# Performance work log

Hardware: AMD Instinct MI355X
Metric: run time of the kernel (lower is better)

The kernel has to match this reference:

```python
import jax, jax.numpy as jnp
import numpy as np

C = 192
NUM_HEADS = 4
K = 3
KV_STRIDE = 2
EPS = 1e-5


def _conv(x, w, stride, groups):
    # x: [B,C,H,W], w: [O, I//groups, kh, kw]
    return jax.lax.conv_general_dilated(
        x, w, window_strides=(stride, stride),
        padding=[(K // 2, K // 2), (K // 2, K // 2)] if w.shape[-1] > 1 else [(0, 0), (0, 0)],
        dimension_numbers=("NCHW", "OIHW", "NCHW"),
        feature_group_count=groups)


def _bn(x, gamma, beta, mean, var):
    # eval-mode batchnorm over channel dim of NCHW
    inv = gamma / jnp.sqrt(var + EPS)
    return x * inv[None, :, None, None] + (beta - mean * inv)[None, :, None, None]


def _dwconv_flatten(x, dw, g, b, m, v, pw, stride):
    y = _conv(x, dw, stride, groups=C)          # depthwise
    y = _bn(y, g, b, m, v)
    y = _conv(y, pw, 1, groups=1)               # 1x1 pointwise
    B, O, h, w = y.shape
    return y.reshape(B, O, h * w).transpose(0, 2, 1)  # b (h w) c


def setup_inputs() -> dict:
    key = jax.random.key(0)
    ks = jax.random.split(key, 16)
    B, H, W = 8, 56, 56
    d = {
        "x": jax.random.normal(ks[0], (B, H * W, C), jnp.float32),
        "H": H,
        "W": W,
        "dw_q": jax.random.normal(ks[1], (C, 1, K, K), jnp.float32) * 0.1,
        "bn_q_gamma": jax.random.uniform(ks[2], (C,), jnp.float32, 0.5, 1.5),
        "bn_q_beta": jax.random.normal(ks[3], (C,), jnp.float32) * 0.1,
        "bn_q_mean": jax.random.normal(ks[4], (C,), jnp.float32) * 0.1,
        "bn_q_var": jax.random.uniform(ks[5], (C,), jnp.float32, 0.5, 1.5),
        "pw_q": jax.random.normal(ks[6], (C, C, 1, 1), jnp.float32) * (1.0 / np.sqrt(C)),
        "dw_kv": jax.random.normal(ks[7], (C, 1, K, K), jnp.float32) * 0.1,
        "bn_kv_gamma": jax.random.uniform(ks[8], (C,), jnp.float32, 0.5, 1.5),
        "bn_kv_beta": jax.random.normal(ks[9], (C,), jnp.float32) * 0.1,
        "bn_kv_mean": jax.random.normal(ks[10], (C,), jnp.float32) * 0.1,
        "bn_kv_var": jax.random.uniform(ks[11], (C,), jnp.float32, 0.5, 1.5),
        "pw_kv": jax.random.normal(ks[12], (2 * C, C, 1, 1), jnp.float32) * (1.0 / np.sqrt(C)),
        "Wq": jax.random.normal(ks[13], (C, C), jnp.float32) * (1.0 / np.sqrt(C)),
        "bq": jnp.zeros((C,), jnp.float32),
        "Wk": jax.random.normal(ks[14], (C, C), jnp.float32) * (1.0 / np.sqrt(C)),
        "bk": jnp.zeros((C,), jnp.float32),
        "Wv": jax.random.normal(ks[15], (C, C), jnp.float32) * (1.0 / np.sqrt(C)),
        "bv": jnp.zeros((C,), jnp.float32),
    }
    return d


def reference(x, H, W, dw_q, bn_q_gamma, bn_q_beta, bn_q_mean, bn_q_var, pw_q,
              dw_kv, bn_kv_gamma, bn_kv_beta, bn_kv_mean, bn_kv_var, pw_kv,
              Wq, bq, Wk, bk, Wv, bv):
    B, N, _ = x.shape
    h = NUM_HEADS
    hd = C // h
    scale = hd ** -0.5
    # Token2Patch: b (H W) c -> b c H W
    xp = x.transpose(0, 2, 1).reshape(B, C, H, W)
    conv_q = _dwconv_flatten(xp, dw_q, bn_q_gamma, bn_q_beta, bn_q_mean, bn_q_var, pw_q, 1)  # [B,N,C]
    kv = _dwconv_flatten(xp, dw_kv, bn_kv_gamma, bn_kv_beta, bn_kv_mean, bn_kv_var, pw_kv, KV_STRIDE)  # [B,M,2C]
    conv_k, conv_v = kv[..., :C], kv[..., C:]
    q = (conv_q @ Wq.T + bq).reshape(B, N, h, hd).transpose(0, 2, 1, 3)      # [B,h,N,hd]
    M = conv_k.shape[1]
    k = (conv_k @ Wk.T + bk).reshape(B, M, h, hd).transpose(0, 2, 1, 3)      # [B,h,M,hd]
    v = (conv_v @ Wv.T + bv).reshape(B, M, h, hd).transpose(0, 2, 1, 3)      # [B,h,M,hd]
    attn = jnp.einsum("bhnd,bhmd->bhnm", q, k) * scale
    attn = jax.nn.softmax(attn, axis=-1)
    out = jnp.einsum("bhnm,bhmd->bhnd", attn, v)
    # MergeHeads: b h n d -> b n (h d)
    return out.transpose(0, 2, 1, 3).reshape(B, N, C)
```

## Files before the change

kernel.cpp:

```cpp
#include <hip/hip_runtime.h>
#include <cmath>

typedef _Float16 f16;
typedef _Float16 f16x8 __attribute__((ext_vector_type(8)));
typedef _Float16 f16x4 __attribute__((ext_vector_type(4)));
typedef float    f32x4 __attribute__((ext_vector_type(4)));
typedef unsigned int u32;
typedef u32 u32x2 __attribute__((ext_vector_type(2)));

#define C_   192
#define HH   56
#define WW   56
#define NN   3136
#define BB   8
#define MM   784
#define NHEAD 4
#define HD   48
#define VT_LD 832
#define QPB  (BB*NN/32)
#define KVPB (BB*MM/32)

#define MFMA16(a,b,c)  __builtin_amdgcn_mfma_f32_16x16x32_f16(a,b,c,0,0,0)
#define MFMAK16(a,b,c) __builtin_amdgcn_mfma_f32_16x16x16f16(a,b,c,0,0,0)

static __device__ __forceinline__ u32 pkrtz(float a, float b) {
    typedef __fp16 fp16x2 __attribute__((ext_vector_type(2)));
    fp16x2 h = __builtin_amdgcn_cvt_pkrtz(a, b);
    return __builtin_bit_cast(u32, h);
}

static __device__ __forceinline__ void gload16(const void* g, void* l) {
    __builtin_amdgcn_global_load_lds(
        (const __attribute__((address_space(1))) unsigned int*)g,
        (__attribute__((address_space(3))) unsigned int*)l, 16, 0, 0);
}

template<int STRIDE, int OH, int OW>
__device__ __forceinline__ void dwbn_quad(
    const float* __restrict__ x, const float* __restrict__ dwL,
    const float* __restrict__ gamma, const float* __restrict__ beta,
    const float* __restrict__ mean,  const float* __restrict__ var,
    f16* __restrict__ out, int idx)
{
    int c4 = idx % 48;
    int r1 = idx / 48;
    int qx = r1 % (OW/2);
    int r2 = r1 / (OW/2);
    int qp = r2 % (OH/2);
    int b  = r2 / (OH/2);
    int c0 = c4*4;

    float4 w4[9];
    #pragma unroll
    for (int j = 0; j < 9; ++j)
        w4[j] = *(const float4*)&dwL[c4*40 + j*4];
    const float* wf = (const float*)w4;

    float4 g4  = *(const float4*)(gamma + c0);
    float4 be4 = *(const float4*)(beta + c0);
    float4 m4  = *(const float4*)(mean + c0);
    float4 v4  = *(const float4*)(var  + c0);

    float4 a00 = make_float4(0.f,0.f,0.f,0.f);
    float4 a01 = a00, a10 = a00, a11 = a00;
    int iyTop = (2*qp)*STRIDE - 1;
    int ix0   = (2*qx)*STRIDE - 1;
    #pragma unroll
    for (int j = 0; j < STRIDE+3; ++j) {
        int iy = iyTop + j;
        if (iy < 0 || iy >= HH) continue;
        #pragma unroll
        for (int i = 0; i < STRIDE+3; ++i) {
            int ix = ix0 + i;
            if (ix < 0 || ix >= WW) continue;
            float4 xv = *reinterpret_cast<const float4*>(
                x + ((size_t)b*NN + iy*WW + ix)*C_ + c0);
            const bool r0ok = (j <= 2), r1ok = (j >= STRIDE);
            const bool c0ok = (i <= 2), c1ok = (i >= STRIDE);
            if (r0ok && c0ok) { const int wi = j*3 + i;
                a00.x = fmaf(wf[ 0+wi], xv.x, a00.x);
                a00.y = fmaf(wf[ 9+wi], xv.y, a00.y);
                a00.z = fmaf(wf[18+wi], xv.z, a00.z);
                a00.w = fmaf(wf[27+wi], xv.w, a00.w); }
            if (r0ok && c1ok) { const int wi = j*3 + (i-STRIDE);
                a01.x = fmaf(wf[ 0+wi], xv.x, a01.x);
                a01.y = fmaf(wf[ 9+wi], xv.y, a01.y);
                a01.z = fmaf(wf[18+wi], xv.z, a01.z);
                a01.w = fmaf(wf[27+wi], xv.w, a01.w); }
            if (r1ok && c0ok) { const int wi = (j-STRIDE)*3 + i;
                a10.x = fmaf(wf[ 0+wi], xv.x, a10.x);
                a10.y = fmaf(wf[ 9+wi], xv.y, a10.y);
                a10.z = fmaf(wf[18+wi], xv.z, a10.z);
                a10.w = fmaf(wf[27+wi], xv.w, a10.w); }
            if (r1ok && c1ok) { const int wi = (j-STRIDE)*3 + (i-STRIDE);
                a11.x = fmaf(wf[ 0+wi], xv.x, a11.x);
                a11.y = fmaf(wf[ 9+wi], xv.y, a11.y);
                a11.z = fmaf(wf[18+wi], xv.z, a11.z);
                a11.w = fmaf(wf[27+wi], xv.w, a11.w); }
        }
    }
    float i0 = g4.x*__frsqrt_rn(v4.x + 1e-5f);
    float i1 = g4.y*__frsqrt_rn(v4.y + 1e-5f);
    float i2 = g4.z*__frsqrt_rn(v4.z + 1e-5f);
    float i3 = g4.w*__frsqrt_rn(v4.w + 1e-5f);
    float b0 = be4.x - m4.x*i0, b1 = be4.y - m4.y*i1;
    float b2 = be4.z - m4.z*i2, b3 = be4.w - m4.w*i3;
    size_t base = (((size_t)b*OH + 2*qp)*OW + 2*qx)*48 + c4;
    f16x4 r;
    r[0]=(f16)(a00.x*i0+b0); r[1]=(f16)(a00.y*i1+b1);
    r[2]=(f16)(a00.z*i2+b2); r[3]=(f16)(a00.w*i3+b3);
    *reinterpret_cast<f16x4*>(out + base*4) = r;
    r[0]=(f16)(a01.x*i0+b0); r[1]=(f16)(a01.y*i1+b1);
    r[2]=(f16)(a01.z*i2+b2); r[3]=(f16)(a01.w*i3+b3);
    *reinterpret_cast<f16x4*>(out + (base + 48)*4) = r;
    r[0]=(f16)(a10.x*i0+b0); r[1]=(f16)(a10.y*i1+b1);
    r[2]=(f16)(a10.z*i2+b2); r[3]=(f16)(a10.w*i3+b3);
    *reinterpret_cast<f16x4*>(out + (base + (size_t)OW*48)*4) = r;
    r[0]=(f16)(a11.x*i0+b0); r[1]=(f16)(a11.y*i1+b1);
    r[2]=(f16)(a11.z*i2+b2); r[3]=(f16)(a11.w*i3+b3);
    *reinterpret_cast<f16x4*>(out + (base + (size_t)OW*48 + 48)*4) = r;
}

__global__ __launch_bounds__(256) void prep_all(
    const float* __restrict__ x,
    const float* __restrict__ dwq,  const float* __restrict__ gq,
    const float* __restrict__ bq_,  const float* __restrict__ mq,
    const float* __restrict__ vq,
    const float* __restrict__ dwkv, const float* __restrict__ gkv,
    const float* __restrict__ bkv,  const float* __restrict__ mkv,
    const float* __restrict__ vkv,
    const float* __restrict__ Wq, const float* __restrict__ Wk,
    const float* __restrict__ Wv, const float* __restrict__ pw_q,
    const float* __restrict__ pw_kv,
    f16* __restrict__ uq, f16* __restrict__ ukv,
    f16* __restrict__ Mq, f16* __restrict__ Mk, f16* __restrict__ Mv,
    f16* __restrict__ vt)
{
    int blk = blockIdx.x, tid = threadIdx.x;
    const int QB = 1176, KB = 294;
    if (blk < QB + KB) {
        bool qp = blk < QB;
        __shared__ __align__(16) float dwL[48*40];
        const float* dwg = qp ? dwq : dwkv;
        for (int i = tid; i < 432; i += 256) {
            int f  = i*4;
            int c4 = f/36, r = f%36;
            *(float4*)&dwL[c4*40 + r] = *(const float4*)(dwg + f);
        }
        __syncthreads();
        if (qp)
            dwbn_quad<1, HH, WW>(x, dwL, gq, bq_, mq, vq, uq, blk*256 + tid);
        else
            dwbn_quad<2, 28, 28>(x, dwL, gkv, bkv, mkv, vkv, ukv,
                                 (blk - QB)*256 + tid);
    } else if (blk < QB + KB + 576) {
        int fb = blk - QB - KB;
        int which = fb / 192, o = fb % 192;
        const float* Wm = which == 0 ? Wq : (which == 1 ? Wk : Wv);
        const float* P  = which == 0 ? pw_q : (which == 1 ? pw_kv : pw_kv + C_*C_);
        f16* Mo         = which == 0 ? Mq : (which == 1 ? Mk : Mv);
        __shared__ float wrow[C_];
        if (tid < C_) wrow[tid] = Wm[o*C_ + tid];
        __syncthreads();
        if (tid < C_) {
            float acc = 0.f;
            #pragma unroll 8
            for (int j = 0; j < C_; ++j)
                acc = fmaf(wrow[j], P[j*C_ + tid], acc);
            Mo[o*C_ + tid] = (f16)acc;
        }
    } else {
        int i = (blk - QB - KB - 576)*256 + tid;
        int b = i / (C_*48);
        int rem = i % (C_*48);
        int c = rem / 48;
        int m = MM + (rem % 48);
        vt[((size_t)b*C_ + c)*VT_LD + m] = (f16)0.f;
    }
}

__global__ __launch_bounds__(128, 1) void proj_all(
    const f16* __restrict__ uq, const f16* __restrict__ ukv,
    const f16* __restrict__ Mq, const f16* __restrict__ Mk,
    const f16* __restrict__ Mv,
    const float* __restrict__ bq, const float* __restrict__ bk,
    const float* __restrict__ bv,
    f16* __restrict__ qb, f16* __restrict__ kb, f16* __restrict__ vt)
{
    int tid  = threadIdx.x;
    int w    = tid >> 6, l = tid & 63;
    int lrow = l & 15,  lgrp = l >> 4;
    int blk  = blockIdx.x;
    int path = blk < QPB ? 0 : (blk < QPB + KVPB ? 1 : 2);
    const f16* U = path == 0 ? uq : ukv;
    int rblk = path == 0 ? blk : (path == 1 ? blk - QPB : blk - QPB - KVPB);
    int r0 = rblk*32 + w*16;

    const f16* urow = U + (size_t)(r0 + lrow)*C_;
    f16x8 a[6];
    #pragma unroll
    for (int ch = 0; ch < 6; ++ch)
        a[ch] = *(const f16x8*)(urow + ch*32 + lgrp*8);

    f16x8 bfA[6], bfB[6];
    const f16* Mm = path == 0 ? Mq : (path == 1 ? Mk : Mv);

    #pragma unroll
    for (int ch = 0; ch < 6; ++ch)
        bfA[ch] = *(const f16x8*)(Mm + (size_t)lrow*C_ + ch*32 + lgrp*8);

    if (path < 2) {
        const float sc = path == 0 ? 0.14433756729740643f*1.4426950408889634f
                                   : 1.0f;
        const float* bias = path == 0 ? bq : bk;
        f16* dst = path == 0 ? qb : kb;
        #pragma unroll
        for (int ct = 0; ct < 12; ++ct) {
            f16x8* cur = (ct & 1) ? bfB : bfA;
            f16x8* nxt = (ct & 1) ? bfA : bfB;
            if (ct < 11) {
                const f16* mrow = Mm + (size_t)((ct+1)*16 + lrow)*C_;
                #pragma unroll
                for (int ch = 0; ch < 6; ++ch)
                    nxt[ch] = *(const f16x8*)(mrow + ch*32 + lgrp*8);
            }
            f32x4 acc = {0.f,0.f,0.f,0.f};
            #pragma unroll
            for (int ch = 0; ch < 6; ++ch)
                acc = MFMA16(cur[ch], a[ch], acc);
            float4 bo = *(const float4*)(bias + ct*16 + lgrp*4);
            f16x4 st;
            st[0] = (f16)((acc[0] + bo.x)*sc);
            st[1] = (f16)((acc[1] + bo.y)*sc);
            st[2] = (f16)((acc[2] + bo.z)*sc);
            st[3] = (f16)((acc[3] + bo.w)*sc);
            *(f16x4*)(dst + (size_t)(r0 + lrow)*C_ + ct*16 + lgrp*4) = st;
        }
    } else {
        #pragma unroll
        for (int ct = 0; ct < 12; ++ct) {
            f16x8* cur = (ct & 1) ? bfB : bfA;
            f16x8* nxt = (ct & 1) ? bfA : bfB;
            if (ct < 11) {
                const f16* mrow = Mv + (size_t)((ct+1)*16 + lrow)*C_;
                #pragma unroll
                for (int ch = 0; ch < 6; ++ch)
                    nxt[ch] = *(const f16x8*)(mrow + ch*32 + lgrp*8);
            }
            int o = ct*16 + lrow;
            f32x4 acc = {0.f,0.f,0.f,0.f};
            #pragma unroll
            for (int ch = 0; ch < 6; ++ch)
                acc = MFMA16(a[ch], cur[ch], acc);
            float bo = bv[o];
            int rg = r0 + lgrp*4;
            int b  = rg / MM, m = rg % MM;
            f16x4 st;
            st[0] = (f16)(acc[0] + bo);
            st[1] = (f16)(acc[1] + bo);
            st[2] = (f16)(acc[2] + bo);
            st[3] = (f16)(acc[3] + bo);
            *(f16x4*)(vt + ((size_t)b*C_ + o)*VT_LD + m) = st;
        }
    }
}

__device__ __forceinline__ void stage_tile(
    int w, int l, f16* ldsKb, f16* ldsVb,
    const f16* __restrict__ kbb, const f16* __restrict__ vbb, int m0)
{
    int rr = l >> 3, p = l & 7;
    #pragma unroll
    for (int j = 0; j < 4; ++j) {
        int u = w + j*4;
        if (u < 8) {
            int r = u*8 + rr;
            int c = p ^ (r & 7);
            gload16(kbb + (size_t)(m0 + r)*C_ + c*8, ldsKb + u*512);
        } else if (u < 14) {
            int d = (u-8)*8 + rr;
            int c = p ^ (d & 7);
            gload16(vbb + (size_t)d*VT_LD + m0 + c*8, ldsVb + (u-8)*512);
        }
    }
}

__device__ __forceinline__ float softmax_upd(
    f32x4* s, float& mrun, float& lrun, u32* pk)
{
    float t0 = fmaxf(fmaxf(s[0][0], s[0][1]), fmaxf(s[0][2], s[0][3]));
    float t1 = fmaxf(fmaxf(s[1][0], s[1][1]), fmaxf(s[1][2], s[1][3]));
    float t2 = fmaxf(fmaxf(s[2][0], s[2][1]), fmaxf(s[2][2], s[2][3]));
    float t3 = fmaxf(fmaxf(s[3][0], s[3][1]), fmaxf(s[3][2], s[3][3]));
    float tmax = fmaxf(fmaxf(t0, t1), fmaxf(t2, t3));
    tmax = fmaxf(tmax, __shfl_xor(tmax, 16));
    tmax = fmaxf(tmax, __shfl_xor(tmax, 32));
    float mnew = fmaxf(mrun, tmax);
    float corr = exp2f(mrun - mnew);
    mrun = mnew;
    float psum = 0.f;
    #pragma unroll
    for (int j = 0; j < 4; ++j) {
        #pragma unroll
        for (int r = 0; r < 4; ++r) {
            s[j][r] = exp2f(s[j][r] - mnew);
            psum += s[j][r];
        }
    }
    lrun = lrun*corr + psum;
    #pragma unroll
    for (int j = 0; j < 4; ++j) {
        pk[j*2]   = pkrtz(s[j][0], s[j][1]);
        pk[j*2+1] = pkrtz(s[j][2], s[j][3]);
    }
    return corr;
}

__device__ __forceinline__ void compute_tile64(
    const f16* ldsKb, const f16* ldsVb,
    const f16x8& qf0, const f16x4& qfh,
    float& mrun, float& lrun, f32x4& o0, f32x4& o1, f32x4& o2,
    int lrow, int g, bool tail)
{
    const char* kP = (const char*)ldsKb;
    const char* vP = (const char*)ldsVb;
    f32x4 z = {0.f,0.f,0.f,0.f};
    int sw = lrow & 7;
    int cA = (g ^ sw) << 4;
    int cH = (((4 + (g >> 1)) ^ sw) << 4) + ((g & 1) << 3);

    f32x4 s[4];
    __builtin_amdgcn_s_setprio(1);
    #pragma unroll
    for (int j = 0; j < 4; ++j) {
        const char* rb = kP + (16*j + lrow)*128;
        f32x4 t = MFMA16(*(const f16x8*)(rb + cA), qf0, z);
        s[j] = MFMAK16(*(const f16x4*)(rb + cH), qfh, t);
    }
    __builtin_amdgcn_s_setprio(0);

    if (tail) {
        f32x4 neg = {-1e30f,-1e30f,-1e30f,-1e30f};
        s[1] = neg; s[2] = neg; s[3] = neg;
    }

    u32 pk[8];
    float corr = softmax_upd(s, mrun, lrun, pk);

    #pragma unroll
    for (int r = 0; r < 4; ++r) { o0[r] *= corr; o1[r] *= corr; o2[r] *= corr; }

    #pragma unroll
    for (int ch = 0; ch < 4; ++ch) {
        u32x2 pw = { pk[2*ch], pk[2*ch+1] };
        f16x4 pb = __builtin_bit_cast(f16x4, pw);
        int off = (((2*ch + (g >> 1)) ^ sw) << 4) + ((g & 1) << 3);
        f16x4 v0 = *(const f16x4*)(vP + lrow*128      + off);
        f16x4 v1 = *(const f16x4*)(vP + (16+lrow)*128 + off);
        f16x4 v2 = *(const f16x4*)(vP + (32+lrow)*128 + off);
        __builtin_amdgcn_s_setprio(1);
        o0 = MFMAK16(v0, pb, o0);
        o1 = MFMAK16(v1, pb, o1);
        o2 = MFMAK16(v2, pb, o2);
        __builtin_amdgcn_s_setprio(0);
    }
}

__global__ __launch_bounds__(256, 4) void attn_mfma(
    const f16* __restrict__ qb, const f16* __restrict__ kb,
    const f16* __restrict__ vt, float* __restrict__ out)
{
    __shared__ __align__(16) f16 ldsK[2][64*64];
    __shared__ __align__(16) f16 ldsV[2][48*64];

    int tid  = threadIdx.x;
    int w    = tid >> 6, l = tid & 63;
    int lrow = l & 15,  g = l >> 4;
    int swz  = (blockIdx.x & 7)*196 + (blockIdx.x >> 3);
    int bh   = swz / 49, qblk = swz % 49;
    int h    = bh & 3, b = bh >> 2;
    int n0   = qblk*64 + w*16;

    const f16* kbb = kb + (size_t)b*MM*C_ + h*HD;
    const f16* vbb = vt + ((size_t)b*C_ + h*HD)*VT_LD;

    const f16* qrow = qb + ((size_t)b*NN + n0 + lrow)*C_ + h*HD;
    f16x8 qf0 = *(const f16x8*)(qrow + g*8);
    f16x4 qfh = *(const f16x4*)(qrow + 32 + g*4);
    asm volatile("" :: "v"(qf0), "v"(qfh));

    float mrun = -1e30f, lrun = 0.f;
    f32x4 o0 = {0.f,0.f,0.f,0.f}, o1 = o0, o2 = o0;

    stage_tile(w, l, &ldsK[0][0], &ldsV[0][0], kbb, vbb, 0);

    for (int t = 0; t < 13; ++t) {
        int nb = t & 1;
        if (t < 12)
            stage_tile(w, l, &ldsK[nb^1][0], &ldsV[nb^1][0], kbb, vbb, (t+1)*64);
        __builtin_amdgcn_sched_barrier(0);
        if (t < 12) {
            if (w < 2) asm volatile("s_waitcnt vmcnt(4)" ::: "memory");
            else       asm volatile("s_waitcnt vmcnt(3)" ::: "memory");
        } else {
            asm volatile("s_waitcnt vmcnt(0)" ::: "memory");
        }
        __builtin_amdgcn_s_barrier();
        __builtin_amdgcn_sched_barrier(0);
        compute_tile64(&ldsK[nb][0], &ldsV[nb][0], qf0, qfh,
                       mrun, lrun, o0, o1, o2, lrow, g, t == 12);
        __builtin_amdgcn_sched_barrier(0);
        __builtin_amdgcn_s_barrier();
    }

    lrun += __shfl_xor(lrun, 16);
    lrun += __shfl_xor(lrun, 32);
    float inv = 1.f / lrun;
    f32x4 r0, r1, r2;
    #pragma unroll
    for (int r = 0; r < 4; ++r) {
        r0[r] = o0[r]*inv; r1[r] = o1[r]*inv; r2[r] = o2[r]*inv;
    }
    float* obase = out + ((size_t)b*NN + n0 + lrow)*C_ + h*HD + g*4;
    *(f32x4*)(obase)      = r0;
    *(f32x4*)(obase + 16) = r1;
    *(f32x4*)(obase + 32) = r2;
}

extern "C" void kernel_launch(void* const* d_in, const int* in_sizes, int n_in,
                              void* d_out, int out_size, void* d_ws, size_t ws_size,
                              hipStream_t stream)
{
    const float* x     = (const float*)d_in[0];
    const float* dw_q  = (const float*)d_in[3];
    const float* bnqg  = (const float*)d_in[4];
    const float* bnqb  = (const float*)d_in[5];
    const float* bnqm  = (const float*)d_in[6];
    const float* bnqv  = (const float*)d_in[7];
    const float* pw_q  = (const float*)d_in[8];
    const float* dw_kv = (const float*)d_in[9];
    const float* bnkg  = (const float*)d_in[10];
    const float* bnkb  = (const float*)d_in[11];
    const float* bnkm  = (const float*)d_in[12];
    const float* bnkvv = (const float*)d_in[13];
    const float* pw_kv = (const float*)d_in[14];
    const float* Wq    = (const float*)d_in[15];
    const float* bq    = (const float*)d_in[16];
    const float* Wk    = (const float*)d_in[17];
    const float* bk    = (const float*)d_in[18];
    const float* Wv    = (const float*)d_in[19];
    const float* bv    = (const float*)d_in[20];
    float* out = (float*)d_out;

    f16* p   = (f16*)d_ws;
    f16* Mq16  = p;  p += C_*C_;
    f16* Mk16  = p;  p += C_*C_;
    f16* Mv16  = p;  p += C_*C_;
    f16* uq16  = p;  p += (size_t)BB*NN*C_;
    f16* ukv16 = p;  p += (size_t)BB*MM*C_;
    f16* qb16  = p;  p += (size_t)BB*NN*C_ + 256;
    f16* kb16  = p;  p += (size_t)BB*MM*C_ + 16384;
    f16* vt16  = p;  p += (size_t)BB*C_*VT_LD;

    prep_all<<<2334, 256, 0, stream>>>(
        x, dw_q, bnqg, bnqb, bnqm, bnqv,
        dw_kv, bnkg, bnkb, bnkm, bnkvv,
        Wq, Wk, Wv, pw_q, pw_kv,
        uq16, ukv16, Mq16, Mk16, Mv16, vt16);

    proj_all<<<QPB + 2*KVPB, 128, 0, stream>>>(
        uq16, ukv16, Mq16, Mk16, Mv16, bq, bk, bv, qb16, kb16, vt16);

    attn_mfma<<<1568, 256, 0, stream>>>(qb16, kb16, vt16, out);
}
```

Baseline: 104.3 us.

## Fuse Q projection into attention kernel, drop separate q buffer

The Q projection GEMM moves out of the projection kernel and into the attention kernel's prologue. Each wave computes its 16x48 head slice of Q from uq with MFMA, applies bias and scale, and passes it through LDS to get the fragment layout. This removes writing and re-reading the full q buffer and shrinks the projection launch. The cost is that each Q tile row is recomputed per head (C×48 per head, no redundancy beyond reading uq once per head), and the kernel's occupancy hint drops from 4 to 2 blocks, which may reduce latency hiding.

```diff
diff --git a/kernel.cpp b/kernel.cpp
--- a/kernel.cpp
+++ b/kernel.cpp
@@ -17,7 +17,6 @@
 #define NHEAD 4
 #define HD   48
 #define VT_LD 832
-#define QPB  (BB*NN/32)
 #define KVPB (BB*MM/32)
 
 #define MFMA16(a,b,c)  __builtin_amdgcn_mfma_f32_16x16x32_f16(a,b,c,0,0,0)
@@ -179,41 +178,34 @@
     }
 }
 
-__global__ __launch_bounds__(128, 1) void proj_all(
-    const f16* __restrict__ uq, const f16* __restrict__ ukv,
-    const f16* __restrict__ Mq, const f16* __restrict__ Mk,
-    const f16* __restrict__ Mv,
-    const float* __restrict__ bq, const float* __restrict__ bk,
-    const float* __restrict__ bv,
-    f16* __restrict__ qb, f16* __restrict__ kb, f16* __restrict__ vt)
+__global__ __launch_bounds__(128, 1) void proj_kv(
+    const f16* __restrict__ ukv,
+    const f16* __restrict__ Mk, const f16* __restrict__ Mv,
+    const float* __restrict__ bk, const float* __restrict__ bv,
+    f16* __restrict__ kb, f16* __restrict__ vt)
 {
     int tid  = threadIdx.x;
     int w    = tid >> 6, l = tid & 63;
     int lrow = l & 15,  lgrp = l >> 4;
     int blk  = blockIdx.x;
-    int path = blk < QPB ? 0 : (blk < QPB + KVPB ? 1 : 2);
-    const f16* U = path == 0 ? uq : ukv;
-    int rblk = path == 0 ? blk : (path == 1 ? blk - QPB : blk - QPB - KVPB);
+    int path = blk < KVPB ? 1 : 2;
+    int rblk = path == 1 ? blk : blk - KVPB;
     int r0 = rblk*32 + w*16;
 
-    const f16* urow = U + (size_t)(r0 + lrow)*C_;
+    const f16* urow = ukv + (size_t)(r0 + lrow)*C_;
     f16x8 a[6];
     #pragma unroll
     for (int ch = 0; ch < 6; ++ch)
         a[ch] = *(const f16x8*)(urow + ch*32 + lgrp*8);
 
     f16x8 bfA[6], bfB[6];
-    const f16* Mm = path == 0 ? Mq : (path == 1 ? Mk : Mv);
+    const f16* Mm = path == 1 ? Mk : Mv;
 
     #pragma unroll
     for (int ch = 0; ch < 6; ++ch)
         bfA[ch] = *(const f16x8*)(Mm + (size_t)lrow*C_ + ch*32 + lgrp*8);
 
-    if (path < 2) {
-        const float sc = path == 0 ? 0.14433756729740643f*1.4426950408889634f
-                                   : 1.0f;
-        const float* bias = path == 0 ? bq : bk;
-        f16* dst = path == 0 ? qb : kb;
+    if (path == 1) {
         #pragma unroll
         for (int ct = 0; ct < 12; ++ct) {
             f16x8* cur = (ct & 1) ? bfB : bfA;
@@ -228,13 +220,13 @@
             #pragma unroll
             for (int ch = 0; ch < 6; ++ch)
                 acc = MFMA16(cur[ch], a[ch], acc);
-            float4 bo = *(const float4*)(bias + ct*16 + lgrp*4);
+            float4 bo = *(const float4*)(bk + ct*16 + lgrp*4);
             f16x4 st;
-            st[0] = (f16)((acc[0] + bo.x)*sc);
-            st[1] = (f16)((acc[1] + bo.y)*sc);
-            st[2] = (f16)((acc[2] + bo.z)*sc);
-            st[3] = (f16)((acc[3] + bo.w)*sc);
-            *(f16x4*)(dst + (size_t)(r0 + lrow)*C_ + ct*16 + lgrp*4) = st;
+            st[0] = (f16)(acc[0] + bo.x);
+            st[1] = (f16)(acc[1] + bo.y);
+            st[2] = (f16)(acc[2] + bo.z);
+            st[3] = (f16)(acc[3] + bo.w);
+            *(f16x4*)(kb + (size_t)(r0 + lrow)*C_ + ct*16 + lgrp*4) = st;
         }
     } else {
         #pragma unroll
@@ -366,12 +358,15 @@
     }
 }
 
-__global__ __launch_bounds__(256, 4) void attn_mfma(
-    const f16* __restrict__ qb, const f16* __restrict__ kb,
-    const f16* __restrict__ vt, float* __restrict__ out)
+__global__ __launch_bounds__(256, 2) void attn_mfma(
+    const f16* __restrict__ uq, const f16* __restrict__ Mq,
+    const float* __restrict__ bq,
+    const f16* __restrict__ kb, const f16* __restrict__ vt,
+    float* __restrict__ out)
 {
     __shared__ __align__(16) f16 ldsK[2][64*64];
     __shared__ __align__(16) f16 ldsV[2][48*64];
+    __shared__ __align__(16) f16 qL[4][16*56];
 
     int tid  = threadIdx.x;
     int w    = tid >> 6, l = tid & 63;
@@ -384,15 +379,38 @@
     const f16* kbb = kb + (size_t)b*MM*C_ + h*HD;
     const f16* vbb = vt + ((size_t)b*C_ + h*HD)*VT_LD;
 
-    const f16* qrow = qb + ((size_t)b*NN + n0 + lrow)*C_ + h*HD;
-    f16x8 qf0 = *(const f16x8*)(qrow + g*8);
-    f16x4 qfh = *(const f16x4*)(qrow + 32 + g*4);
+    stage_tile(w, l, &ldsK[0][0], &ldsV[0][0], kbb, vbb, 0);
+
+    {
+        const float qsc = 0.14433756729740643f * 1.4426950408889634f;
+        f16* qw = &qL[w][0];
+        const f16* urow = uq + ((size_t)b*NN + n0 + lrow)*C_;
+        f16x8 ufr[6];
+        #pragma unroll
+        for (int ch = 0; ch < 6; ++ch)
+            ufr[ch] = *(const f16x8*)(urow + ch*32 + g*8);
+        #pragma unroll
+        for (int dt = 0; dt < 3; ++dt) {
+            const f16* mrow = Mq + (size_t)(h*HD + dt*16 + lrow)*C_;
+            f32x4 acc = {0.f,0.f,0.f,0.f};
+            #pragma unroll
+            for (int ch = 0; ch < 6; ++ch)
+                acc = MFMA16(*(const f16x8*)(mrow + ch*32 + g*8), ufr[ch], acc);
+            float4 bo = *(const float4*)(bq + h*HD + dt*16 + g*4);
+            f16x4 st;
+            st[0] = (f16)((acc[0] + bo.x)*qsc);
+            st[1] = (f16)((acc[1] + bo.y)*qsc);
+            st[2] = (f16)((acc[2] + bo.z)*qsc);
+            st[3] = (f16)((acc[3] + bo.w)*qsc);
+            *(f16x4*)(qw + lrow*56 + dt*16 + g*4) = st;
+        }
+    }
+    f16x8 qf0 = *(const f16x8*)(&qL[w][0] + lrow*56 + g*8);
+    f16x4 qfh = *(const f16x4*)(&qL[w][0] + lrow*56 + 32 + g*4);
     asm volatile("" :: "v"(qf0), "v"(qfh));
 
     float mrun = -1e30f, lrun = 0.f;
     f32x4 o0 = {0.f,0.f,0.f,0.f}, o1 = o0, o2 = o0;
-
-    stage_tile(w, l, &ldsK[0][0], &ldsV[0][0], kbb, vbb, 0);
 
     for (int t = 0; t < 13; ++t) {
         int nb = t & 1;
@@ -456,9 +474,8 @@
     f16* Mq16  = p;  p += C_*C_;
     f16* Mk16  = p;  p += C_*C_;
     f16* Mv16  = p;  p += C_*C_;
-    f16* uq16  = p;  p += (size_t)BB*NN*C_;
+    f16* uq16  = p;  p += (size_t)BB*NN*C_ + 256;
     f16* ukv16 = p;  p += (size_t)BB*MM*C_;
-    f16* qb16  = p;  p += (size_t)BB*NN*C_ + 256;
     f16* kb16  = p;  p += (size_t)BB*MM*C_ + 16384;
     f16* vt16  = p;  p += (size_t)BB*C_*VT_LD;
 
@@ -468,8 +485,8 @@
         Wq, Wk, Wv, pw_q, pw_kv,
         uq16, ukv16, Mq16, Mk16, Mv16, vt16);
 
-    proj_all<<<QPB + 2*KVPB, 128, 0, stream>>>(
-        uq16, ukv16, Mq16, Mk16, Mv16, bq, bk, bv, qb16, kb16, vt16);
-
-    attn_mfma<<<1568, 256, 0, stream>>>(qb16, kb16, vt16, out);
-}
+    proj_kv<<<2*KVPB, 128, 0, stream>>>(
+        ukv16, Mk16, Mv16, bk, bv, kb16, vt16);
+
+    attn_mfma<<<1568, 256, 0, stream>>>(uq16, Mq16, bq, kb16, vt16, out);
+}
```

New measurement: 100.4 us. 3.7% less time.
